# Performance work log

Hardware: AMD Instinct MI355X
Metric: run time of the kernel (lower is better)

Reference implementation:

```python
import jax, jax.numpy as jnp
import numpy as np

V, P, TY, D, H, L, B, T = 30522, 512, 2, 768, 12, 12, 8, 512
DF = 4 * D


def layer_norm(x, g, b, eps=1e-5):
    m = jnp.mean(x, axis=-1, keepdims=True)
    v = jnp.var(x, axis=-1, keepdims=True)
    return (x - m) * jax.lax.rsqrt(v + eps) * g + b


def new_gelu(x):
    c = np.sqrt(2.0 / np.pi).astype(np.float32)
    return 0.5 * x * (1.0 + jnp.tanh(c * (x + 0.044715 * x * x * x)))


def setup_inputs() -> dict:
    key = jax.random.key(0)
    ks = jax.random.split(key, 10)
    s = 0.02
    n = lambda k, shape: (jax.random.normal(k, shape, jnp.float32) * s)
    return dict(
        input_ids=jax.random.randint(ks[0], (B, T), 0, V),
        token_type_ids=jax.random.randint(ks[1], (B, T), 0, TY),
        attention_mask=jnp.ones((B, T), jnp.float32),
        word_emb=n(ks[2], (V, D)),
        pos_emb=n(ks[3], (P, D)),
        type_emb=n(ks[4], (TY, D)),
        emb_ln_g=jnp.ones((D,), jnp.float32), emb_ln_b=jnp.zeros((D,), jnp.float32),
        ln1_g=jnp.ones((L, D), jnp.float32), ln1_b=jnp.zeros((L, D), jnp.float32),
        wqkv=n(ks[5], (L, D, 3 * D)), bqkv=jnp.zeros((L, 3 * D), jnp.float32),
        wproj=n(ks[6], (L, D, D)) / np.sqrt(2 * L).astype(np.float32),
        bproj=jnp.zeros((L, D), jnp.float32),
        ln2_g=jnp.ones((L, D), jnp.float32), ln2_b=jnp.zeros((L, D), jnp.float32),
        wfc=n(ks[7], (L, D, DF)), bfc=jnp.zeros((L, DF), jnp.float32),
        wfc2=n(ks[8], (L, DF, D)) / np.sqrt(2 * L).astype(np.float32),
        bfc2=jnp.zeros((L, D), jnp.float32),
    )


def reference(input_ids, token_type_ids, attention_mask, word_emb, pos_emb, type_emb,
              emb_ln_g, emb_ln_b, ln1_g, ln1_b, wqkv, bqkv, wproj, bproj,
              ln2_g, ln2_b, wfc, bfc, wfc2, bfc2):
    Bx, Tx = input_ids.shape
    hd = D // H
    scale = np.float32(1.0 / np.sqrt(hd))
    # embeddings: word + position + token-type, then LayerNorm (dropout = 0)
    x = word_emb[input_ids] + pos_emb[:Tx][None, :, :] + type_emb[token_type_ids]
    x = layer_norm(x, emb_ln_g, emb_ln_b)
    # additive mask bias, broadcast over heads and query positions: [B,1,1,T]
    mask_bias = (1.0 - attention_mask)[:, None, None, :] * (-10000.0)

    def block(x, p):
        l1g, l1b, wq, bq, wp, bp, l2g, l2b, wf, bf, w2, b2 = p
        h = layer_norm(x, l1g, l1b)
        qkv = h @ wq + bq                                   # [B,T,3D]
        q, k, v = jnp.split(qkv, 3, axis=-1)
        q = q.reshape(Bx, Tx, H, hd).transpose(0, 2, 1, 3)  # [B,H,T,hd]
        k = k.reshape(Bx, Tx, H, hd).transpose(0, 2, 1, 3)
        v = v.reshape(Bx, Tx, H, hd).transpose(0, 2, 1, 3)
        att = jnp.einsum('bhqd,bhkd->bhqk', q, k) * scale + mask_bias
        att = jax.nn.softmax(att, axis=-1)
        y = jnp.einsum('bhqk,bhkd->bhqd', att, v)
        y = y.transpose(0, 2, 1, 3).reshape(Bx, Tx, D)
        x = x + (y @ wp + bp)                               # attn residual
        h2 = layer_norm(x, l2g, l2b)
        h2 = new_gelu(h2 @ wf + bf) @ w2 + b2               # GELU MLP
        return x + h2, None

    x, _ = jax.lax.scan(block, x, (ln1_g, ln1_b, wqkv, bqkv, wproj, bproj,
                                   ln2_g, ln2_b, wfc, bfc, wfc2, bfc2))
    # baseline MLM head: weight tied to word embeddings, no bias
    logits = x @ word_emb.T                                 # [B,T,V]
    return logits
```

## Files before the change

kernel.cpp:

```cpp
#include <hip/hip_runtime.h>
#include <hip/hip_bf16.h>

typedef unsigned short u16;
typedef __attribute__((ext_vector_type(4))) float f32x4;
typedef __attribute__((ext_vector_type(8))) __bf16 bf16x8;

#define DEV static __device__ __forceinline__

DEV float b2f(u16 v) { return __uint_as_float(((unsigned)v) << 16); }

DEV u16 f2b(float f) {
  unsigned u = __float_as_uint(f);
  return (u16)((u + 0x7fffu + ((u >> 16) & 1u)) >> 16);
}

DEV void gload16(const void* g, void* l) {
  __builtin_amdgcn_global_load_lds(
      (__attribute__((address_space(1))) void*)g,
      (__attribute__((address_space(3))) void*)l, 16, 0, 0);
}

DEV float wave_sum(float v) {
  #pragma unroll
  for (int o = 32; o; o >>= 1) v += __shfl_xor(v, o, 64);
  return v;
}

__global__ __launch_bounds__(256)
void embed_ln_k(const int* __restrict__ ids, const int* __restrict__ tts,
                const float* __restrict__ we, const float* __restrict__ pe,
                const float* __restrict__ te, const float* __restrict__ g,
                const float* __restrict__ bb, float* __restrict__ x) {
  const int t = blockIdx.x;
  const int pos = t & 511;
  const int tid = threadIdx.x, lane = tid & 63, w = tid >> 6;
  const int id = ids[t], tt = tts[t];
  __shared__ float red[8];
  float e[3];
  #pragma unroll
  for (int k = 0; k < 3; k++) {
    int d = tid + k * 256;
    e[k] = we[(size_t)id * 768 + d] + pe[(size_t)pos * 768 + d] + te[(size_t)tt * 768 + d];
  }
  float s = wave_sum(e[0] + e[1] + e[2]);
  if (lane == 0) red[w] = s;
  __syncthreads();
  const float mean = (red[0] + red[1] + red[2] + red[3]) * (1.f / 768.f);
  float v2 = 0.f;
  #pragma unroll
  for (int k = 0; k < 3; k++) { float d = e[k] - mean; v2 += d * d; }
  v2 = wave_sum(v2);
  if (lane == 0) red[4 + w] = v2;
  __syncthreads();
  const float var = (red[4] + red[5] + red[6] + red[7]) * (1.f / 768.f);
  const float rstd = rsqrtf(var + 1e-5f);
  #pragma unroll
  for (int k = 0; k < 3; k++) {
    int d = tid + k * 256;
    x[(size_t)t * 768 + d] = (e[k] - mean) * rstd * g[d] + bb[d];
  }
}

__global__ __launch_bounds__(256)
void ln_k(const float* __restrict__ xin, const float* __restrict__ g,
          const float* __restrict__ bb, u16* __restrict__ out) {
  const int t = blockIdx.x;
  const int tid = threadIdx.x, lane = tid & 63, w = tid >> 6;
  __shared__ float red[8];
  float e[3];
  #pragma unroll
  for (int k = 0; k < 3; k++) e[k] = xin[(size_t)t * 768 + tid + k * 256];
  float s = wave_sum(e[0] + e[1] + e[2]);
  if (lane == 0) red[w] = s;
  __syncthreads();
  const float mean = (red[0] + red[1] + red[2] + red[3]) * (1.f / 768.f);
  float v2 = 0.f;
  #pragma unroll
  for (int k = 0; k < 3; k++) { float d = e[k] - mean; v2 += d * d; }
  v2 = wave_sum(v2);
  if (lane == 0) red[4 + w] = v2;
  __syncthreads();
  const float var = (red[4] + red[5] + red[6] + red[7]) * (1.f / 768.f);
  const float rstd = rsqrtf(var + 1e-5f);
  #pragma unroll
  for (int k = 0; k < 3; k++) {
    int d = tid + k * 256;
    out[(size_t)t * 768 + d] = f2b((e[k] - mean) * rstd * g[d] + bb[d]);
  }
}

__global__ __launch_bounds__(256)
void cast_k(const float* __restrict__ xin, u16* __restrict__ out) {
  const int i = blockIdx.x * 256 + threadIdx.x;
  float4 v = ((const float4*)xin)[i];
  uint2 o;
  o.x = (unsigned)f2b(v.x) | ((unsigned)f2b(v.y) << 16);
  o.y = (unsigned)f2b(v.z) | ((unsigned)f2b(v.w) << 16);
  ((uint2*)out)[i] = o;
}

__global__ __launch_bounds__(256)
void wecast_k(const float* __restrict__ we, u16* __restrict__ out) {
  const int i = blockIdx.x * 256 + threadIdx.x;
  const int row = i / 96, c8 = i % 96;
  uint2 o0 = make_uint2(0u, 0u), o1 = make_uint2(0u, 0u);
  if (row < 30522) {
    const float* src = we + (size_t)row * 768 + c8 * 8;
    float4 a = ((const float4*)src)[0];
    float4 b = ((const float4*)src)[1];
    o0.x = (unsigned)f2b(a.x) | ((unsigned)f2b(a.y) << 16);
    o0.y = (unsigned)f2b(a.z) | ((unsigned)f2b(a.w) << 16);
    o1.x = (unsigned)f2b(b.x) | ((unsigned)f2b(b.y) << 16);
    o1.y = (unsigned)f2b(b.z) | ((unsigned)f2b(b.w) << 16);
  }
  uint2* dst = (uint2*)(out + (size_t)i * 8);
  dst[0] = o0;
  dst[1] = o1;
}

DEV void tconv_tile(const float* __restrict__ W, u16* __restrict__ Wt,
                    int K, int N, int n0, int k0, int tid, u16 (*t)[65]) {
  const int kl = tid >> 4, nl4 = (tid & 15) * 4;
  #pragma unroll
  for (int i = 0; i < 4; i++) {
    float4 v = *(const float4*)(W + (size_t)(k0 + kl + i * 16) * N + n0 + nl4);
    t[nl4 + 0][kl + i * 16] = f2b(v.x);
    t[nl4 + 1][kl + i * 16] = f2b(v.y);
    t[nl4 + 2][kl + i * 16] = f2b(v.z);
    t[nl4 + 3][kl + i * 16] = f2b(v.w);
  }
  __syncthreads();
  const int nl = tid >> 2, kc = (tid & 3) * 16;
  unsigned wd[8];
  #pragma unroll
  for (int j = 0; j < 8; j++)
    wd[j] = (unsigned)t[nl][kc + 2 * j] | ((unsigned)t[nl][kc + 2 * j + 1] << 16);
  int4* dst = (int4*)(Wt + (size_t)(n0 + nl) * K + k0 + kc);
  dst[0] = make_int4((int)wd[0], (int)wd[1], (int)wd[2], (int)wd[3]);
  dst[1] = make_int4((int)wd[4], (int)wd[5], (int)wd[6], (int)wd[7]);
}

__global__ __launch_bounds__(256)
void tconv_k(const float* __restrict__ W, u16* __restrict__ Wt, int K, int N) {
  __shared__ u16 t[64][65];
  tconv_tile(W, Wt, K, N, blockIdx.x * 64, blockIdx.y * 64, threadIdx.x, t);
}

__global__ __launch_bounds__(256)
void tconv_all_k(const float* __restrict__ wqkv, const float* __restrict__ wprj,
                 const float* __restrict__ wfc, const float* __restrict__ wfc2,
                 u16* __restrict__ wall) {
  __shared__ u16 ts[64][65];
  const int tile = blockIdx.x;
  const int l = tile / 1728, t = tile % 1728;
  u16* base = wall + (size_t)l * 7077888;
  const float* W; u16* Wt; int K, N, loc;
  if (t < 432)       { W = wqkv + (size_t)l * 768 * 2304; Wt = base;           K = 768;  N = 2304; loc = t; }
  else if (t < 576)  { W = wprj + (size_t)l * 768 * 768;  Wt = base + 1769472; K = 768;  N = 768;  loc = t - 432; }
  else if (t < 1152) { W = wfc  + (size_t)l * 768 * 3072; Wt = base + 2359296; K = 768;  N = 3072; loc = t - 576; }
  else               { W = wfc2 + (size_t)l * 3072 * 768; Wt = base + 4718592; K = 3072; N = 768;  loc = t - 1152; }
  const int nbl = N >> 6;
  tconv_tile(W, Wt, K, N, (loc % nbl) * 64, (loc / nbl) * 64, threadIdx.x, ts);
}

template <int EPI>
__global__ __launch_bounds__(256)
void gemm_k(const u16* __restrict__ A, const u16* __restrict__ B,
            const float* __restrict__ bias, const float* __restrict__ resid,
            void* __restrict__ Cptr, int Ndim, int Kdim, int Nblk) {
  __shared__ __align__(16) u16 As[2][128 * 32];
  __shared__ __align__(16) u16 Bs[2][128 * 32];
  const int tid = threadIdx.x, lane = tid & 63, w = tid >> 6;
  const int wr = w >> 1, wc = w & 1, fr = lane & 15, fq = lane >> 4;

  const int nwg = gridDim.x, chunk = nwg >> 3;
  const int tile = (blockIdx.x & 7) * chunk + (blockIdx.x >> 3);
  const int nb = tile % Nblk, mb = tile / Nblk;
  const int n0 = nb * 128, m0 = mb * 128;

  f32x4 acc[4][4] = {};
  const int arow = w * 16 + (lane >> 2), akk = (lane & 3) * 8;

  for (int k0 = 0; k0 < Kdim; k0 += 64) {
    #pragma unroll
    for (int kh = 0; kh < 2; kh++) {
      const int kk = k0 + kh * 32 + akk;
      gload16(A + (size_t)(m0 + arow) * Kdim + kk,      &As[kh][w * 512]);
      gload16(A + (size_t)(m0 + 64 + arow) * Kdim + kk, &As[kh][2048 + w * 512]);
      gload16(B + (size_t)(n0 + arow) * Kdim + kk,      &Bs[kh][w * 512]);
      gload16(B + (size_t)(n0 + 64 + arow) * Kdim + kk, &Bs[kh][2048 + w * 512]);
    }
    __syncthreads();
    #pragma unroll
    for (int kh = 0; kh < 2; kh++) {
      bf16x8 af[4], bfv[4];
      #pragma unroll
      for (int m = 0; m < 4; m++)
        af[m] = *(const bf16x8*)(&As[kh][(wr * 64 + m * 16 + fr) * 32 + fq * 8]);
      #pragma unroll
      for (int n = 0; n < 4; n++)
        bfv[n] = *(const bf16x8*)(&Bs[kh][(wc * 64 + n * 16 + fr) * 32 + fq * 8]);
      #pragma unroll
      for (int m = 0; m < 4; m++)
        #pragma unroll
        for (int n = 0; n < 4; n++)
          acc[m][n] = __builtin_amdgcn_mfma_f32_16x16x32_bf16(af[m], bfv[n], acc[m][n], 0, 0, 0);
    }
    __syncthreads();
  }

  #pragma unroll
  for (int m = 0; m < 4; m++) {
    const int row = m0 + wr * 64 + m * 16 + fq * 4;
    #pragma unroll
    for (int n = 0; n < 4; n++) {
      const int col = n0 + wc * 64 + n * 16 + fr;
      if (EPI == 3 && col >= Ndim) continue;
      const float bv = (bias != nullptr) ? bias[col] : 0.f;
      #pragma unroll
      for (int r = 0; r < 4; r++) {
        float v = acc[m][n][r] + bv;
        const size_t idx = (size_t)(row + r) * Ndim + col;
        if (EPI == 0) {
          ((u16*)Cptr)[idx] = f2b(v);
        } else if (EPI == 1) {
          float t = v;
          float gl = 0.5f * t * (1.f + tanhf(0.7978845608f * (t + 0.044715f * t * t * t)));
          ((u16*)Cptr)[idx] = f2b(gl);
        } else if (EPI == 2) {
          ((float*)Cptr)[idx] = resid[idx] + v;
        } else {
          ((float*)Cptr)[idx] = v;
        }
      }
    }
  }
}

template <int EPI>
__global__ __launch_bounds__(256)
void gemm64_k(const u16* __restrict__ A, const u16* __restrict__ B,
              const float* __restrict__ bias, const float* __restrict__ resid,
              void* __restrict__ Cptr, int Ndim, int Kdim, int Nblk) {
  __shared__ __align__(16) u16 As[2][64 * 32];
  __shared__ __align__(16) u16 Bs[2][64 * 32];
  const int tid = threadIdx.x, lane = tid & 63, w = tid >> 6;
  const int wr = w >> 1, wc = w & 1, fr = lane & 15, fq = lane >> 4;

  const int nwg = gridDim.x, chunk = nwg >> 3;
  const int tile = (blockIdx.x & 7) * chunk + (blockIdx.x >> 3);
  const int nb = tile % Nblk, mb = tile / Nblk;
  const int n0 = nb * 64, m0 = mb * 64;

  f32x4 acc[2][2] = {};
  const int arow = w * 16 + (lane >> 2), akk = (lane & 3) * 8;

  for (int k0 = 0; k0 < Kdim; k0 += 64) {
    #pragma unroll
    for (int kh = 0; kh < 2; kh++) {
      const int kk = k0 + kh * 32 + akk;
      gload16(A + (size_t)(m0 + arow) * Kdim + kk, &As[kh][w * 512]);
      gload16(B + (size_t)(n0 + arow) * Kdim + kk, &Bs[kh][w * 512]);
    }
    __syncthreads();
    #pragma unroll
    for (int kh = 0; kh < 2; kh++) {
      bf16x8 af[2], bfv[2];
      #pragma unroll
      for (int m = 0; m < 2; m++)
        af[m] = *(const bf16x8*)(&As[kh][(wr * 32 + m * 16 + fr) * 32 + fq * 8]);
      #pragma unroll
      for (int n = 0; n < 2; n++)
        bfv[n] = *(const bf16x8*)(&Bs[kh][(wc * 32 + n * 16 + fr) * 32 + fq * 8]);
      #pragma unroll
      for (int m = 0; m < 2; m++)
        #pragma unroll
        for (int n = 0; n < 2; n++)
          acc[m][n] = __builtin_amdgcn_mfma_f32_16x16x32_bf16(af[m], bfv[n], acc[m][n], 0, 0, 0);
    }
    __syncthreads();
  }

  #pragma unroll
  for (int m = 0; m < 2; m++) {
    const int row = m0 + wr * 32 + m * 16 + fq * 4;
    #pragma unroll
    for (int n = 0; n < 2; n++) {
      const int col = n0 + wc * 32 + n * 16 + fr;
      const float bv = (bias != nullptr) ? bias[col] : 0.f;
      #pragma unroll
      for (int r = 0; r < 4; r++) {
        float v = acc[m][n][r] + bv;
        const size_t idx = (size_t)(row + r) * Ndim + col;
        if (EPI == 0) {
          ((u16*)Cptr)[idx] = f2b(v);
        } else if (EPI == 1) {
          float t = v;
          float gl = 0.5f * t * (1.f + tanhf(0.7978845608f * (t + 0.044715f * t * t * t)));
          ((u16*)Cptr)[idx] = f2b(gl);
        } else if (EPI == 2) {
          ((float*)Cptr)[idx] = resid[idx] + v;
        } else {
          ((float*)Cptr)[idx] = v;
        }
      }
    }
  }
}

__global__ __launch_bounds__(256)
void attn_mfma_k(const u16* __restrict__ qkv, const float* __restrict__ amask,
                 u16* __restrict__ y) {
  __shared__ __align__(16) u16 Ks[2][64 * 64];
  __shared__ __align__(16) u16 Vt[2][64 * 64];
  __shared__ __align__(16) u16 Ps[4][16 * 64];
  const int tid = threadIdx.x, lane = tid & 63, w = tid >> 6;
  const int bh = blockIdx.y, b = bh / 12, hh = bh % 12;
  const int q0 = blockIdx.x * 64;
  const u16* qb = qkv + (size_t)(b * 512) * 2304 + hh * 64;
  const u16* kb = qb + 768;
  const u16* vb = qb + 1536;
  const int fr = lane & 15, fq = lane >> 4;

  bf16x8 af[2];
  {
    const u16* qrow = qb + (size_t)(q0 + w * 16 + fr) * 2304;
    af[0] = *(const bf16x8*)(qrow + fq * 8);
    af[1] = *(const bf16x8*)(qrow + 32 + fq * 8);
  }

  auto stageK = [&](int kt, int nb) {
    const int r0 = lane >> 3, dc = lane & 7, s = dc ^ r0;
    #pragma unroll
    for (int p = 0; p < 2; p++) {
      const int i = w * 2 + p;
      gload16(kb + (size_t)(kt * 64 + i * 8 + r0) * 2304 + s * 8,
              (void*)&Ks[nb][i * 512]);
    }
  };
  auto stageV = [&](int kt, int nb) {
    #pragma unroll
    for (int p = 0; p < 2; p++) {
      const int dc = w * 2 + p;
      int4 vd = *(const int4*)(vb + (size_t)(kt * 64 + lane) * 2304 + dc * 8);
      union { int4 v; u16 e[8]; } u; u.v = vd;
      #pragma unroll
      for (int ii = 0; ii < 8; ii++)
        Vt[nb][(dc * 8 + ii) * 64 + (lane ^ (ii << 3))] = u.e[ii];
    }
  };

  f32x4 O[4];
  #pragma unroll
  for (int nd = 0; nd < 4; nd++) O[nd] = f32x4{0.f, 0.f, 0.f, 0.f};
  float run_m[4], run_l[4];
  #pragma unroll
  for (int r = 0; r < 4; r++) { run_m[r] = -3.0e38f; run_l[r] = 0.f; }

  stageK(0, 0); stageV(0, 0);
  __syncthreads();
  int cur = 0;

  for (int kt = 0; kt < 8; kt++) {
    if (kt < 7) { stageK(kt + 1, cur ^ 1); stageV(kt + 1, cur ^ 1); }

    bf16x8 kf[4][2];
    #pragma unroll
    for (int n = 0; n < 4; n++)
      #pragma unroll
      for (int kh = 0; kh < 2; kh++)
        kf[n][kh] = *(const bf16x8*)(&Ks[cur][(n * 16 + fr) * 64 + ((kh * 4 + fq) ^ (fr & 7)) * 8]);
    f32x4 sacc[4];
    #pragma unroll
    for (int n = 0; n < 4; n++) sacc[n] = f32x4{0.f, 0.f, 0.f, 0.f};
    #pragma unroll
    for (int n = 0; n < 4; n++)
      #pragma unroll
      for (int kh = 0; kh < 2; kh++)
        sacc[n] = __builtin_amdgcn_mfma_f32_16x16x32_bf16(af[kh], kf[n][kh], sacc[n], 0, 0, 0);

    float mb[4];
    #pragma unroll
    for (int n = 0; n < 4; n++)
      mb[n] = (1.0f - amask[b * 512 + kt * 64 + n * 16 + fr]) * -10000.0f;
    float s[4][4];
    #pragma unroll
    for (int n = 0; n < 4; n++)
      #pragma unroll
      for (int r = 0; r < 4; r++) s[n][r] = sacc[n][r] * 0.125f + mb[n];
    float tm[4];
    #pragma unroll
    for (int r = 0; r < 4; r++) {
      tm[r] = fmaxf(fmaxf(s[0][r], s[1][r]), fmaxf(s[2][r], s[3][r]));
      #pragma unroll
      for (int o = 1; o < 16; o <<= 1) tm[r] = fmaxf(tm[r], __shfl_xor(tm[r], o, 64));
    }
    float al[4], ts[4];
    float p[4][4];
    #pragma unroll
    for (int r = 0; r < 4; r++) {
      float nm = fmaxf(run_m[r], tm[r]);
      al[r] = __expf(run_m[r] - nm);
      run_m[r] = nm;
      ts[r] = 0.f;
      #pragma unroll
      for (int n = 0; n < 4; n++) { p[n][r] = __expf(s[n][r] - nm); ts[r] += p[n][r]; }
      #pragma unroll
      for (int o = 1; o < 16; o <<= 1) ts[r] += __shfl_xor(ts[r], o, 64);
      run_l[r] = run_l[r] * al[r] + ts[r];
    }
    #pragma unroll
    for (int nd = 0; nd < 4; nd++)
      #pragma unroll
      for (int r = 0; r < 4; r++) O[nd][r] *= al[r];

    #pragma unroll
    for (int n = 0; n < 4; n++)
      #pragma unroll
      for (int r = 0; r < 4; r++) {
        const int q = fq * 4 + r, j = n * 16 + fr;
        Ps[w][q * 64 + (j ^ ((q & 7) << 3))] = f2b(p[n][r]);
      }
    asm volatile("s_waitcnt lgkmcnt(0)" ::: "memory");
    __builtin_amdgcn_sched_barrier(0);

    bf16x8 pa[2];
    #pragma unroll
    for (int kh = 0; kh < 2; kh++)
      pa[kh] = *(const bf16x8*)(&Ps[w][fr * 64 + ((kh * 4 + fq) ^ (fr & 7)) * 8]);
    #pragma unroll
    for (int nd = 0; nd < 4; nd++) {
      bf16x8 vf0 = *(const bf16x8*)(&Vt[cur][(nd * 16 + fr) * 64 + ((0 + fq) ^ (fr & 7)) * 8]);
      bf16x8 vf1 = *(const bf16x8*)(&Vt[cur][(nd * 16 + fr) * 64 + ((4 + fq) ^ (fr & 7)) * 8]);
      O[nd] = __builtin_amdgcn_mfma_f32_16x16x32_bf16(pa[0], vf0, O[nd], 0, 0, 0);
      O[nd] = __builtin_amdgcn_mfma_f32_16x16x32_bf16(pa[1], vf1, O[nd], 0, 0, 0);
    }
    __syncthreads();
    cur ^= 1;
  }

  float inv[4];
  #pragma unroll
  for (int r = 0; r < 4; r++) inv[r] = 1.0f / run_l[r];
  #pragma unroll
  for (int nd = 0; nd < 4; nd++)
    #pragma unroll
    for (int r = 0; r < 4; r++) {
      const int q = q0 + w * 16 + fq * 4 + r;
      y[(size_t)(b * 512 + q) * 768 + hh * 64 + nd * 16 + fr] = f2b(O[nd][r] * inv[r]);
    }
}

extern "C" void kernel_launch(void* const* d_in, const int* in_sizes, int n_in,
                              void* d_out, int out_size, void* d_ws, size_t ws_size,
                              hipStream_t stream) {
  (void)in_sizes; (void)n_in; (void)out_size;
  const int*   ids  = (const int*)d_in[0];
  const int*   tts  = (const int*)d_in[1];
  const float* am   = (const float*)d_in[2];
  const float* we   = (const float*)d_in[3];
  const float* pe   = (const float*)d_in[4];
  const float* te   = (const float*)d_in[5];
  const float* eg   = (const float*)d_in[6];
  const float* eb   = (const float*)d_in[7];
  const float* l1g  = (const float*)d_in[8];
  const float* l1b  = (const float*)d_in[9];
  const float* wqkv = (const float*)d_in[10];
  const float* bqkv = (const float*)d_in[11];
  const float* wprj = (const float*)d_in[12];
  const float* bprj = (const float*)d_in[13];
  const float* l2g  = (const float*)d_in[14];
  const float* l2b  = (const float*)d_in[15];
  const float* wfc  = (const float*)d_in[16];
  const float* bfc  = (const float*)d_in[17];
  const float* wfc2 = (const float*)d_in[18];
  const float* bfc2 = (const float*)d_in[19];

  char* ws = (char*)d_ws;
  float* x   = (float*)ws;
  u16*  h    = (u16*)(ws + 12582912);
  u16*  qkv  = (u16*)(ws + 18874368);
  u16*  y    = (u16*)(ws + 37748736);
  u16*  fc   = (u16*)(ws + 18874368);
  u16*  we_b = (u16*)(ws + 44040192);
  u16*  wall = (u16*)(ws + 91029504);
  const bool upfront = ws_size >= 260898816ull;
  u16* wqkv_f = (u16*)(ws + 91029504);
  u16* wprj_f = wqkv_f + 1769472;
  u16* wfc_f  = wqkv_f + 2359296;
  u16* wfc2_f = wqkv_f + 4718592;

  wecast_k<<<11472, 256, 0, stream>>>(we, we_b);
  embed_ln_k<<<4096, 256, 0, stream>>>(ids, tts, we, pe, te, eg, eb, x);
  if (upfront)
    tconv_all_k<<<20736, 256, 0, stream>>>(wqkv, wprj, wfc, wfc2, wall);

  for (int l = 0; l < 12; l++) {
    u16 *wq_b, *wp_b, *wf_b, *w2_b;
    if (upfront) {
      u16* base = wall + (size_t)l * 7077888;
      wq_b = base; wp_b = base + 1769472; wf_b = base + 2359296; w2_b = base + 4718592;
    } else {
      tconv_k<<<dim3(36, 12), 256, 0, stream>>>(wqkv + (size_t)l * 768 * 2304, wqkv_f, 768, 2304);
      tconv_k<<<dim3(12, 12), 256, 0, stream>>>(wprj + (size_t)l * 768 * 768,  wprj_f, 768, 768);
      tconv_k<<<dim3(48, 12), 256, 0, stream>>>(wfc  + (size_t)l * 768 * 3072, wfc_f,  768, 3072);
      tconv_k<<<dim3(12, 48), 256, 0, stream>>>(wfc2 + (size_t)l * 3072 * 768, wfc2_f, 3072, 768);
      wq_b = wqkv_f; wp_b = wprj_f; wf_b = wfc_f; w2_b = wfc2_f;
    }

    ln_k<<<4096, 256, 0, stream>>>(x, l1g + l * 768, l1b + l * 768, h);
    gemm_k<0><<<576, 256, 0, stream>>>(
        h, wq_b, bqkv + l * 2304, nullptr, qkv, 2304, 768, 18);
    attn_mfma_k<<<dim3(8, 96), 256, 0, stream>>>(qkv, am, y);
    gemm64_k<2><<<768, 256, 0, stream>>>(
        y, wp_b, bprj + l * 768, x, x, 768, 768, 12);
    ln_k<<<4096, 256, 0, stream>>>(x, l2g + l * 768, l2b + l * 768, h);
    gemm_k<1><<<768, 256, 0, stream>>>(
        h, wf_b, bfc + l * 3072, nullptr, fc, 3072, 768, 24);
    gemm64_k<2><<<768, 256, 0, stream>>>(
        fc, w2_b, bfc2 + l * 768, x, x, 768, 3072, 12);
  }

  cast_k<<<3072, 256, 0, stream>>>(x, h);
  gemm_k<3><<<7648, 256, 0, stream>>>(
      h, we_b, nullptr, nullptr, d_out, 30522, 768, 239);
}
```

Baseline: 2.525 ms.

## Rework LayerNorm, GEMM LDS layout, attention softmax, and add 256-row logits GEMM

LayerNorm now assigns one wave per token with float4 loads and packed bf16 stores, so no block-level barriers are needed. The GEMM kernels stage a full 64-wide K slice into a single XOR-swizzled LDS buffer to reduce bank conflicts. Attention moves the mask bias into LDS and swaps the MFMA operand order so each lane holds one query row, which removes most cross-lane reductions; it also adds setprio hints and vectorised output stores. A new 256x128-tile GEMM handles the large vocabulary projection to raise operand reuse, at the cost of more LDS and registers and possibly lower occupancy.

```diff
diff --git a/kernel.cpp b/kernel.cpp
--- a/kernel.cpp
+++ b/kernel.cpp
@@ -12,6 +12,10 @@
 DEV u16 f2b(float f) {
   unsigned u = __float_as_uint(f);
   return (u16)((u + 0x7fffu + ((u >> 16) & 1u)) >> 16);
+}
+
+DEV unsigned pk2(float a, float b) {
+  return (unsigned)f2b(a) | ((unsigned)f2b(b) << 16);
 }
 
 DEV void gload16(const void* g, void* l) {
@@ -64,28 +68,34 @@
 __global__ __launch_bounds__(256)
 void ln_k(const float* __restrict__ xin, const float* __restrict__ g,
           const float* __restrict__ bb, u16* __restrict__ out) {
-  const int t = blockIdx.x;
-  const int tid = threadIdx.x, lane = tid & 63, w = tid >> 6;
-  __shared__ float red[8];
-  float e[3];
-  #pragma unroll
-  for (int k = 0; k < 3; k++) e[k] = xin[(size_t)t * 768 + tid + k * 256];
-  float s = wave_sum(e[0] + e[1] + e[2]);
-  if (lane == 0) red[w] = s;
-  __syncthreads();
-  const float mean = (red[0] + red[1] + red[2] + red[3]) * (1.f / 768.f);
+  const int lane = threadIdx.x & 63, w = threadIdx.x >> 6;
+  const int t = blockIdx.x * 4 + w;
+  const float4* x4 = (const float4*)(xin + (size_t)t * 768);
+  float4 e[3];
+  #pragma unroll
+  for (int k = 0; k < 3; k++) e[k] = x4[k * 64 + lane];
+  float s = 0.f;
+  #pragma unroll
+  for (int k = 0; k < 3; k++) s += e[k].x + e[k].y + e[k].z + e[k].w;
+  s = wave_sum(s);
+  const float mean = s * (1.f / 768.f);
   float v2 = 0.f;
   #pragma unroll
-  for (int k = 0; k < 3; k++) { float d = e[k] - mean; v2 += d * d; }
+  for (int k = 0; k < 3; k++) {
+    float a = e[k].x - mean, b = e[k].y - mean, c = e[k].z - mean, d = e[k].w - mean;
+    v2 += a * a + b * b + c * c + d * d;
+  }
   v2 = wave_sum(v2);
-  if (lane == 0) red[4 + w] = v2;
-  __syncthreads();
-  const float var = (red[4] + red[5] + red[6] + red[7]) * (1.f / 768.f);
-  const float rstd = rsqrtf(var + 1e-5f);
+  const float rstd = rsqrtf(v2 * (1.f / 768.f) + 1e-5f);
+  uint2* o2 = (uint2*)(out + (size_t)t * 768);
   #pragma unroll
   for (int k = 0; k < 3; k++) {
-    int d = tid + k * 256;
-    out[(size_t)t * 768 + d] = f2b((e[k] - mean) * rstd * g[d] + bb[d]);
+    float4 gv = ((const float4*)g)[k * 64 + lane];
+    float4 bv = ((const float4*)bb)[k * 64 + lane];
+    uint2 o;
+    o.x = pk2((e[k].x - mean) * rstd * gv.x + bv.x, (e[k].y - mean) * rstd * gv.y + bv.y);
+    o.y = pk2((e[k].z - mean) * rstd * gv.z + bv.z, (e[k].w - mean) * rstd * gv.w + bv.w);
+    o2[k * 64 + lane] = o;
   }
 }
 
@@ -94,8 +104,8 @@
   const int i = blockIdx.x * 256 + threadIdx.x;
   float4 v = ((const float4*)xin)[i];
   uint2 o;
-  o.x = (unsigned)f2b(v.x) | ((unsigned)f2b(v.y) << 16);
-  o.y = (unsigned)f2b(v.z) | ((unsigned)f2b(v.w) << 16);
+  o.x = pk2(v.x, v.y);
+  o.y = pk2(v.z, v.w);
   ((uint2*)out)[i] = o;
 }
 
@@ -108,10 +118,8 @@
     const float* src = we + (size_t)row * 768 + c8 * 8;
     float4 a = ((const float4*)src)[0];
     float4 b = ((const float4*)src)[1];
-    o0.x = (unsigned)f2b(a.x) | ((unsigned)f2b(a.y) << 16);
-    o0.y = (unsigned)f2b(a.z) | ((unsigned)f2b(a.w) << 16);
-    o1.x = (unsigned)f2b(b.x) | ((unsigned)f2b(b.y) << 16);
-    o1.y = (unsigned)f2b(b.z) | ((unsigned)f2b(b.w) << 16);
+    o0.x = pk2(a.x, a.y); o0.y = pk2(a.z, a.w);
+    o1.x = pk2(b.x, b.y); o1.y = pk2(b.z, b.w);
   }
   uint2* dst = (uint2*)(out + (size_t)i * 8);
   dst[0] = o0;
@@ -168,8 +176,8 @@
 void gemm_k(const u16* __restrict__ A, const u16* __restrict__ B,
             const float* __restrict__ bias, const float* __restrict__ resid,
             void* __restrict__ Cptr, int Ndim, int Kdim, int Nblk) {
-  __shared__ __align__(16) u16 As[2][128 * 32];
-  __shared__ __align__(16) u16 Bs[2][128 * 32];
+  __shared__ __align__(16) u16 As[128 * 64];
+  __shared__ __align__(16) u16 Bs[128 * 64];
   const int tid = threadIdx.x, lane = tid & 63, w = tid >> 6;
   const int wr = w >> 1, wc = w & 1, fr = lane & 15, fq = lane >> 4;
 
@@ -179,27 +187,27 @@
   const int n0 = nb * 128, m0 = mb * 128;
 
   f32x4 acc[4][4] = {};
-  const int arow = w * 16 + (lane >> 2), akk = (lane & 3) * 8;
+  const int rl = lane >> 3;
+  const int sl = ((lane & 7) ^ rl) * 8;
 
   for (int k0 = 0; k0 < Kdim; k0 += 64) {
     #pragma unroll
+    for (int i = 0; i < 4; i++) {
+      const int row = i * 32 + w * 8 + rl;
+      gload16(A + (size_t)(m0 + row) * Kdim + k0 + sl, As + (i * 32 + w * 8) * 64);
+      gload16(B + (size_t)(n0 + row) * Kdim + k0 + sl, Bs + (i * 32 + w * 8) * 64);
+    }
+    __syncthreads();
+    #pragma unroll
     for (int kh = 0; kh < 2; kh++) {
-      const int kk = k0 + kh * 32 + akk;
-      gload16(A + (size_t)(m0 + arow) * Kdim + kk,      &As[kh][w * 512]);
-      gload16(A + (size_t)(m0 + 64 + arow) * Kdim + kk, &As[kh][2048 + w * 512]);
-      gload16(B + (size_t)(n0 + arow) * Kdim + kk,      &Bs[kh][w * 512]);
-      gload16(B + (size_t)(n0 + 64 + arow) * Kdim + kk, &Bs[kh][2048 + w * 512]);
-    }
-    __syncthreads();
-    #pragma unroll
-    for (int kh = 0; kh < 2; kh++) {
+      const int ks = ((kh * 4 + fq) ^ (fr & 7)) * 8;
       bf16x8 af[4], bfv[4];
       #pragma unroll
       for (int m = 0; m < 4; m++)
-        af[m] = *(const bf16x8*)(&As[kh][(wr * 64 + m * 16 + fr) * 32 + fq * 8]);
+        af[m] = *(const bf16x8*)(&As[(wr * 64 + m * 16 + fr) * 64 + ks]);
       #pragma unroll
       for (int n = 0; n < 4; n++)
-        bfv[n] = *(const bf16x8*)(&Bs[kh][(wc * 64 + n * 16 + fr) * 32 + fq * 8]);
+        bfv[n] = *(const bf16x8*)(&Bs[(wc * 64 + n * 16 + fr) * 64 + ks]);
       #pragma unroll
       for (int m = 0; m < 4; m++)
         #pragma unroll
@@ -215,7 +223,6 @@
     #pragma unroll
     for (int n = 0; n < 4; n++) {
       const int col = n0 + wc * 64 + n * 16 + fr;
-      if (EPI == 3 && col >= Ndim) continue;
       const float bv = (bias != nullptr) ? bias[col] : 0.f;
       #pragma unroll
       for (int r = 0; r < 4; r++) {
@@ -229,8 +236,6 @@
           ((u16*)Cptr)[idx] = f2b(gl);
         } else if (EPI == 2) {
           ((float*)Cptr)[idx] = resid[idx] + v;
-        } else {
-          ((float*)Cptr)[idx] = v;
         }
       }
     }
@@ -242,8 +247,8 @@
 void gemm64_k(const u16* __restrict__ A, const u16* __restrict__ B,
               const float* __restrict__ bias, const float* __restrict__ resid,
               void* __restrict__ Cptr, int Ndim, int Kdim, int Nblk) {
-  __shared__ __align__(16) u16 As[2][64 * 32];
-  __shared__ __align__(16) u16 Bs[2][64 * 32];
+  __shared__ __align__(16) u16 As[64 * 64];
+  __shared__ __align__(16) u16 Bs[64 * 64];
   const int tid = threadIdx.x, lane = tid & 63, w = tid >> 6;
   const int wr = w >> 1, wc = w & 1, fr = lane & 15, fq = lane >> 4;
 
@@ -253,25 +258,27 @@
   const int n0 = nb * 64, m0 = mb * 64;
 
   f32x4 acc[2][2] = {};
-  const int arow = w * 16 + (lane >> 2), akk = (lane & 3) * 8;
+  const int rl = lane >> 3;
+  const int sl = ((lane & 7) ^ rl) * 8;
 
   for (int k0 = 0; k0 < Kdim; k0 += 64) {
     #pragma unroll
+    for (int i = 0; i < 2; i++) {
+      const int row = i * 32 + w * 8 + rl;
+      gload16(A + (size_t)(m0 + row) * Kdim + k0 + sl, As + (i * 32 + w * 8) * 64);
+      gload16(B + (size_t)(n0 + row) * Kdim + k0 + sl, Bs + (i * 32 + w * 8) * 64);
+    }
+    __syncthreads();
+    #pragma unroll
     for (int kh = 0; kh < 2; kh++) {
-      const int kk = k0 + kh * 32 + akk;
-      gload16(A + (size_t)(m0 + arow) * Kdim + kk, &As[kh][w * 512]);
-      gload16(B + (size_t)(n0 + arow) * Kdim + kk, &Bs[kh][w * 512]);
-    }
-    __syncthreads();
-    #pragma unroll
-    for (int kh = 0; kh < 2; kh++) {
+      const int ks = ((kh * 4 + fq) ^ (fr & 7)) * 8;
       bf16x8 af[2], bfv[2];
       #pragma unroll
       for (int m = 0; m < 2; m++)
-        af[m] = *(const bf16x8*)(&As[kh][(wr * 32 + m * 16 + fr) * 32 + fq * 8]);
+        af[m] = *(const bf16x8*)(&As[(wr * 32 + m * 16 + fr) * 64 + ks]);
       #pragma unroll
       for (int n = 0; n < 2; n++)
-        bfv[n] = *(const bf16x8*)(&Bs[kh][(wc * 32 + n * 16 + fr) * 32 + fq * 8]);
+        bfv[n] = *(const bf16x8*)(&Bs[(wc * 32 + n * 16 + fr) * 64 + ks]);
       #pragma unroll
       for (int m = 0; m < 2; m++)
         #pragma unroll
@@ -300,10 +307,70 @@
           ((u16*)Cptr)[idx] = f2b(gl);
         } else if (EPI == 2) {
           ((float*)Cptr)[idx] = resid[idx] + v;
-        } else {
-          ((float*)Cptr)[idx] = v;
         }
       }
+    }
+  }
+}
+
+__global__ __launch_bounds__(256)
+void gemm256_k(const u16* __restrict__ A, const u16* __restrict__ B,
+               float* __restrict__ Cptr, int Ndim, int Kdim, int Nblk) {
+  __shared__ __align__(16) u16 As[256 * 64];
+  __shared__ __align__(16) u16 Bs[128 * 64];
+  const int tid = threadIdx.x, lane = tid & 63, w = tid >> 6;
+  const int fr = lane & 15, fq = lane >> 4;
+
+  const int nwg = gridDim.x, chunk = nwg >> 3;
+  const int tile = (blockIdx.x & 7) * chunk + (blockIdx.x >> 3);
+  const int nb = tile % Nblk, mb = tile / Nblk;
+  const int n0 = nb * 128, m0 = mb * 256;
+
+  f32x4 acc[4][8] = {};
+  const int rl = lane >> 3;
+  const int sl = ((lane & 7) ^ rl) * 8;
+
+  for (int k0 = 0; k0 < Kdim; k0 += 64) {
+    #pragma unroll
+    for (int i = 0; i < 8; i++) {
+      const int row = i * 32 + w * 8 + rl;
+      gload16(A + (size_t)(m0 + row) * Kdim + k0 + sl, As + (i * 32 + w * 8) * 64);
+    }
+    #pragma unroll
+    for (int i = 0; i < 4; i++) {
+      const int row = i * 32 + w * 8 + rl;
+      gload16(B + (size_t)(n0 + row) * Kdim + k0 + sl, Bs + (i * 32 + w * 8) * 64);
+    }
+    __syncthreads();
+    #pragma unroll
+    for (int kh = 0; kh < 2; kh++) {
+      const int ks = ((kh * 4 + fq) ^ (fr & 7)) * 8;
+      bf16x8 af[4], bfv[8];
+      #pragma unroll
+      for (int m = 0; m < 4; m++)
+        af[m] = *(const bf16x8*)(&As[(w * 64 + m * 16 + fr) * 64 + ks]);
+      #pragma unroll
+      for (int n = 0; n < 8; n++)
+        bfv[n] = *(const bf16x8*)(&Bs[(n * 16 + fr) * 64 + ks]);
+      #pragma unroll
+      for (int m = 0; m < 4; m++)
+        #pragma unroll
+        for (int n = 0; n < 8; n++)
+          acc[m][n] = __builtin_amdgcn_mfma_f32_16x16x32_bf16(af[m], bfv[n], acc[m][n], 0, 0, 0);
+    }
+    __syncthreads();
+  }
+
+  #pragma unroll
+  for (int m = 0; m < 4; m++) {
+    const int row = m0 + w * 64 + m * 16 + fq * 4;
+    #pragma unroll
+    for (int n = 0; n < 8; n++) {
+      const int col = n0 + n * 16 + fr;
+      if (col >= Ndim) continue;
+      #pragma unroll
+      for (int r = 0; r < 4; r++)
+        Cptr[(size_t)(row + r) * Ndim + col] = acc[m][n][r];
     }
   }
 }
@@ -314,6 +381,7 @@
   __shared__ __align__(16) u16 Ks[2][64 * 64];
   __shared__ __align__(16) u16 Vt[2][64 * 64];
   __shared__ __align__(16) u16 Ps[4][16 * 64];
+  __shared__ float bias_lds[512];
   const int tid = threadIdx.x, lane = tid & 63, w = tid >> 6;
   const int bh = blockIdx.y, b = bh / 12, hh = bh % 12;
   const int q0 = blockIdx.x * 64;
@@ -322,6 +390,9 @@
   const u16* vb = qb + 1536;
   const int fr = lane & 15, fq = lane >> 4;
 
+  bias_lds[tid] = (1.0f - amask[b * 512 + tid]) * -10000.0f;
+  bias_lds[tid + 256] = (1.0f - amask[b * 512 + tid + 256]) * -10000.0f;
+
   bf16x8 af[2];
   {
     const u16* qrow = qb + (size_t)(q0 + w * 16 + fr) * 2304;
@@ -353,9 +424,7 @@
   f32x4 O[4];
   #pragma unroll
   for (int nd = 0; nd < 4; nd++) O[nd] = f32x4{0.f, 0.f, 0.f, 0.f};
-  float run_m[4], run_l[4];
-  #pragma unroll
-  for (int r = 0; r < 4; r++) { run_m[r] = -3.0e38f; run_l[r] = 0.f; }
+  float run_m = -3.0e38f, run_l = 0.f;
 
   stageK(0, 0); stageV(0, 0);
   __syncthreads();
@@ -364,91 +433,83 @@
   for (int kt = 0; kt < 8; kt++) {
     if (kt < 7) { stageK(kt + 1, cur ^ 1); stageV(kt + 1, cur ^ 1); }
 
-    bf16x8 kf[4][2];
+    f32x4 sacc[4];
+    #pragma unroll
+    for (int n = 0; n < 4; n++) sacc[n] = f32x4{0.f, 0.f, 0.f, 0.f};
+    __builtin_amdgcn_s_setprio(1);
     #pragma unroll
     for (int n = 0; n < 4; n++)
       #pragma unroll
-      for (int kh = 0; kh < 2; kh++)
-        kf[n][kh] = *(const bf16x8*)(&Ks[cur][(n * 16 + fr) * 64 + ((kh * 4 + fq) ^ (fr & 7)) * 8]);
-    f32x4 sacc[4];
-    #pragma unroll
-    for (int n = 0; n < 4; n++) sacc[n] = f32x4{0.f, 0.f, 0.f, 0.f};
+      for (int kh = 0; kh < 2; kh++) {
+        bf16x8 kf = *(const bf16x8*)(&Ks[cur][(n * 16 + fr) * 64 + ((kh * 4 + fq) ^ (fr & 7)) * 8]);
+        sacc[n] = __builtin_amdgcn_mfma_f32_16x16x32_bf16(kf, af[kh], sacc[n], 0, 0, 0);
+      }
+    __builtin_amdgcn_s_setprio(0);
+
+    float s[4][4];
+    float vm = -3.0e38f;
+    #pragma unroll
+    for (int n = 0; n < 4; n++) {
+      float4 b4 = *(const float4*)(&bias_lds[kt * 64 + n * 16 + fq * 4]);
+      s[n][0] = sacc[n][0] * 0.125f + b4.x;
+      s[n][1] = sacc[n][1] * 0.125f + b4.y;
+      s[n][2] = sacc[n][2] * 0.125f + b4.z;
+      s[n][3] = sacc[n][3] * 0.125f + b4.w;
+      vm = fmaxf(vm, fmaxf(fmaxf(s[n][0], s[n][1]), fmaxf(s[n][2], s[n][3])));
+    }
+    vm = fmaxf(vm, __shfl_xor(vm, 16, 64));
+    vm = fmaxf(vm, __shfl_xor(vm, 32, 64));
+    const float nm = fmaxf(run_m, vm);
+    const float al = __expf(run_m - nm);
+    run_m = nm;
+    float p[4][4], ts = 0.f;
     #pragma unroll
     for (int n = 0; n < 4; n++)
       #pragma unroll
-      for (int kh = 0; kh < 2; kh++)
-        sacc[n] = __builtin_amdgcn_mfma_f32_16x16x32_bf16(af[kh], kf[n][kh], sacc[n], 0, 0, 0);
-
-    float mb[4];
-    #pragma unroll
-    for (int n = 0; n < 4; n++)
-      mb[n] = (1.0f - amask[b * 512 + kt * 64 + n * 16 + fr]) * -10000.0f;
-    float s[4][4];
-    #pragma unroll
-    for (int n = 0; n < 4; n++)
-      #pragma unroll
-      for (int r = 0; r < 4; r++) s[n][r] = sacc[n][r] * 0.125f + mb[n];
-    float tm[4];
-    #pragma unroll
-    for (int r = 0; r < 4; r++) {
-      tm[r] = fmaxf(fmaxf(s[0][r], s[1][r]), fmaxf(s[2][r], s[3][r]));
-      #pragma unroll
-      for (int o = 1; o < 16; o <<= 1) tm[r] = fmaxf(tm[r], __shfl_xor(tm[r], o, 64));
-    }
-    float al[4], ts[4];
-    float p[4][4];
-    #pragma unroll
-    for (int r = 0; r < 4; r++) {
-      float nm = fmaxf(run_m[r], tm[r]);
-      al[r] = __expf(run_m[r] - nm);
-      run_m[r] = nm;
-      ts[r] = 0.f;
-      #pragma unroll
-      for (int n = 0; n < 4; n++) { p[n][r] = __expf(s[n][r] - nm); ts[r] += p[n][r]; }
-      #pragma unroll
-      for (int o = 1; o < 16; o <<= 1) ts[r] += __shfl_xor(ts[r], o, 64);
-      run_l[r] = run_l[r] * al[r] + ts[r];
-    }
-    #pragma unroll
-    for (int nd = 0; nd < 4; nd++)
-      #pragma unroll
-      for (int r = 0; r < 4; r++) O[nd][r] *= al[r];
-
-    #pragma unroll
-    for (int n = 0; n < 4; n++)
-      #pragma unroll
-      for (int r = 0; r < 4; r++) {
-        const int q = fq * 4 + r, j = n * 16 + fr;
-        Ps[w][q * 64 + (j ^ ((q & 7) << 3))] = f2b(p[n][r]);
-      }
+      for (int r = 0; r < 4; r++) { p[n][r] = __expf(s[n][r] - nm); ts += p[n][r]; }
+    ts += __shfl_xor(ts, 16, 64);
+    ts += __shfl_xor(ts, 32, 64);
+    run_l = run_l * al + ts;
+    #pragma unroll
+    for (int nd = 0; nd < 4; nd++) O[nd] *= al;
+
+    #pragma unroll
+    for (int n = 0; n < 4; n++) {
+      uint2 dw;
+      dw.x = pk2(p[n][0], p[n][1]);
+      dw.y = pk2(p[n][2], p[n][3]);
+      const int slot = (2 * n + (fq >> 1)) ^ (fr & 7);
+      *(uint2*)((char*)&Ps[w][0] + fr * 128 + slot * 16 + (fq & 1) * 8) = dw;
+    }
     asm volatile("s_waitcnt lgkmcnt(0)" ::: "memory");
     __builtin_amdgcn_sched_barrier(0);
 
-    bf16x8 pa[2];
+    bf16x8 pb[2];
     #pragma unroll
     for (int kh = 0; kh < 2; kh++)
-      pa[kh] = *(const bf16x8*)(&Ps[w][fr * 64 + ((kh * 4 + fq) ^ (fr & 7)) * 8]);
+      pb[kh] = *(const bf16x8*)((char*)&Ps[w][0] + fr * 128 + (((kh * 4 + fq) ^ (fr & 7)) * 16));
+    __builtin_amdgcn_s_setprio(1);
     #pragma unroll
     for (int nd = 0; nd < 4; nd++) {
       bf16x8 vf0 = *(const bf16x8*)(&Vt[cur][(nd * 16 + fr) * 64 + ((0 + fq) ^ (fr & 7)) * 8]);
       bf16x8 vf1 = *(const bf16x8*)(&Vt[cur][(nd * 16 + fr) * 64 + ((4 + fq) ^ (fr & 7)) * 8]);
-      O[nd] = __builtin_amdgcn_mfma_f32_16x16x32_bf16(pa[0], vf0, O[nd], 0, 0, 0);
-      O[nd] = __builtin_amdgcn_mfma_f32_16x16x32_bf16(pa[1], vf1, O[nd], 0, 0, 0);
-    }
+      O[nd] = __builtin_amdgcn_mfma_f32_16x16x32_bf16(vf0, pb[0], O[nd], 0, 0, 0);
+      O[nd] = __builtin_amdgcn_mfma_f32_16x16x32_bf16(vf1, pb[1], O[nd], 0, 0, 0);
+    }
+    __builtin_amdgcn_s_setprio(0);
     __syncthreads();
     cur ^= 1;
   }
 
-  float inv[4];
-  #pragma unroll
-  for (int r = 0; r < 4; r++) inv[r] = 1.0f / run_l[r];
-  #pragma unroll
-  for (int nd = 0; nd < 4; nd++)
-    #pragma unroll
-    for (int r = 0; r < 4; r++) {
-      const int q = q0 + w * 16 + fq * 4 + r;
-      y[(size_t)(b * 512 + q) * 768 + hh * 64 + nd * 16 + fr] = f2b(O[nd][r] * inv[r]);
-    }
+  const float inv = 1.0f / run_l;
+  u16* yrow = y + (size_t)(b * 512 + q0 + w * 16 + fr) * 768 + hh * 64;
+  #pragma unroll
+  for (int nd = 0; nd < 4; nd++) {
+    uint2 o;
+    o.x = pk2(O[nd][0] * inv, O[nd][1] * inv);
+    o.y = pk2(O[nd][2] * inv, O[nd][3] * inv);
+    *(uint2*)(yrow + nd * 16 + fq * 4) = o;
+  }
 }
 
 extern "C" void kernel_launch(void* const* d_in, const int* in_sizes, int n_in,
@@ -508,13 +569,13 @@
       wq_b = wqkv_f; wp_b = wprj_f; wf_b = wfc_f; w2_b = wfc2_f;
     }
 
-    ln_k<<<4096, 256, 0, stream>>>(x, l1g + l * 768, l1b + l * 768, h);
+    ln_k<<<1024, 256, 0, stream>>>(x, l1g + l * 768, l1b + l * 768, h);
     gemm_k<0><<<576, 256, 0, stream>>>(
         h, wq_b, bqkv + l * 2304, nullptr, qkv, 2304, 768, 18);
     attn_mfma_k<<<dim3(8, 96), 256, 0, stream>>>(qkv, am, y);
     gemm64_k<2><<<768, 256, 0, stream>>>(
         y, wp_b, bprj + l * 768, x, x, 768, 768, 12);
-    ln_k<<<4096, 256, 0, stream>>>(x, l2g + l * 768, l2b + l * 768, h);
+    ln_k<<<1024, 256, 0, stream>>>(x, l2g + l * 768, l2b + l * 768, h);
     gemm_k<1><<<768, 256, 0, stream>>>(
         h, wf_b, bfc + l * 3072, nullptr, fc, 3072, 768, 24);
     gemm64_k<2><<<768, 256, 0, stream>>>(
@@ -522,6 +583,6 @@
   }
 
   cast_k<<<3072, 256, 0, stream>>>(x, h);
-  gemm_k<3><<<7648, 256, 0, stream>>>(
-      h, we_b, nullptr, nullptr, d_out, 30522, 768, 239);
-}
+  gemm256_k<<<3824, 256, 0, stream>>>(
+      h, we_b, (float*)d_out, 30522, 768, 239);
+}
```

Measured after the change: 2.425 ms. -4.0%, faster.
